# Optimization experiments

Hardware: AMD Instinct MI355X
Metric: run time of the kernel (lower is better)

The kernel has to match this reference:

```python
import jax, jax.numpy as jnp
import numpy as np

N_LOW, N_HIGH = 8000, 50000
C_IN, R2 = 25, 25
N_L25 = N_LOW * R2
E_LL, E_LH, E_HH = 32000, N_HIGH * 25, N_HIGH * 16
EPS = 1e-5


def _bn(x, g, b):
    # geometric_nn.BatchNorm in train mode: per-batch (per-node-set) stats
    mu = x.mean(0)
    var = x.var(0)
    return (x - mu) * jax.lax.rsqrt(var + EPS) * g + b


def _gcn(x, src, dst, W, b, n):
    # PyG GCNConv (normalize=True, add_self_loops=True) applied per-variable.
    # x: [n, V, C], W: [V, C, O]
    h = jnp.einsum('nvc,vco->nvo', x, W)
    sl = jnp.arange(n, dtype=src.dtype)
    s = jnp.concatenate([src, sl])
    d = jnp.concatenate([dst, sl])
    deg = jax.ops.segment_sum(jnp.ones_like(d, dtype=h.dtype), d, n)
    dis = jax.lax.rsqrt(jnp.maximum(deg, 1.0))
    norm = dis[s] * dis[d]
    out = jax.ops.segment_sum(h[s] * norm[:, None, None], d, n)
    return out + b


def _gatv2(xs, xd, src, dst, Wl, bl, Wr, br, att, bias, heads, oc, n_dst,
           concat, self_loops):
    # PyG GATv2Conv, eval mode (dropout off), aggr='mean'.
    hl = (xs @ Wl + bl).reshape(-1, heads, oc)  # source/messages
    hr = (xd @ Wr + br).reshape(-1, heads, oc)  # target/query
    if self_loops:
        sl = jnp.arange(n_dst, dtype=src.dtype)
        src = jnp.concatenate([src, sl])
        dst = jnp.concatenate([dst, sl])
    e = jax.nn.leaky_relu(hl[src] + hr[dst], 0.2)          # [E,H,C]
    logit = jnp.einsum('ehc,hc->eh', e, att)               # [E,H]
    m = jax.ops.segment_max(logit, dst, n_dst)
    a = jnp.exp(logit - m[dst])
    den = jax.ops.segment_sum(a, dst, n_dst)
    alpha = a / jnp.maximum(den, 1e-16)[dst]               # segment softmax
    msg = alpha[..., None] * hl[src]                       # [E,H,C]
    ssum = jax.ops.segment_sum(msg, dst, n_dst)
    cnt = jax.ops.segment_sum(jnp.ones_like(dst, dtype=ssum.dtype), dst, n_dst)
    out = ssum / jnp.maximum(cnt, 1.0)[:, None, None]      # mean aggregation
    out = out.reshape(n_dst, heads * oc) if concat else out.mean(1)
    return out + bias


def _forward(x_low, z_std, gcn_w, gcn_b, th_wl, th_bl, th_wr, th_br, th_att,
             th_bias, bn0_g, bn0_b, g1_wl, g1_bl, g1_wr, g1_br, g1_att,
             g1_bias, bn_g, bn_b, gm_wl, gm_bl, gm_wr, gm_br, gm_att, gm_bias,
             g5_wl, g5_bl, g5_wr, g5_br, g5_att, g5_bias, p_w1, p_b1, p_w2,
             p_b2, p_w3, p_b3, ei_ll, src_l2h, dst_l2h, ei_hh):
    # 5 GCN downscale branches done together: [N_LOW, 5, 625]
    enc = _gcn(x_low, ei_ll[0], ei_ll[1], gcn_w, gcn_b, N_LOW)
    # PixelShuffle(r=5) on [N,1,625,1,1] -> [N,1,25,5,5]; flatten+permute+cat
    # == reshape to [n, var, chan25, spat25] -> [n, spat25, var, chan25]
    enc = enc.reshape(N_LOW, 5, C_IN, R2).transpose(0, 3, 1, 2)
    enc = enc.reshape(N_L25, 5 * C_IN)                     # [200000, 125]
    h = _gatv2(enc, z_std, src_l2h, dst_l2h, th_wl, th_bl, th_wr, th_br,
               th_att, th_bias, 4, 25, N_HIGH, False, False)
    x = jnp.concatenate([z_std, h], axis=-1)               # [N_HIGH, 26]
    src, dst = ei_hh[0], ei_hh[1]
    x = _bn(x, bn0_g, bn0_b)
    x = _gatv2(x, x, src, dst, g1_wl, g1_bl, g1_wr, g1_br, g1_att, g1_bias,
               2, 64, N_HIGH, True, True)
    for i in range(3):
        x = jax.nn.relu(_bn(x, bn_g[i], bn_b[i]))
        x = _gatv2(x, x, src, dst, gm_wl[i], gm_bl[i], gm_wr[i], gm_br[i],
                   gm_att[i], gm_bias[i], 2, 64, N_HIGH, True, True)
    x = jax.nn.relu(_bn(x, bn_g[3], bn_b[3]))
    x = jax.nn.relu(_gatv2(x, x, src, dst, g5_wl, g5_bl, g5_wr, g5_br,
                           g5_att, g5_bias, 1, 64, N_HIGH, True, True))
    x = jax.nn.relu(x @ p_w1 + p_b1)
    x = jax.nn.relu(x @ p_w2 + p_b2)
    return x @ p_w3 + p_b3                                 # [N_HIGH, 1]


def setup_inputs() -> dict:
    key = jax.random.key(0)
    ks = iter(jax.random.split(key, 64))
    rn = lambda *s: jax.random.normal(next(ks), s, jnp.float32)
    w = lambda *s: rn(*s) * 0.1
    return dict(
        x_low=rn(N_LOW, 5, C_IN),
        z_std=rn(N_HIGH, 1),
        gcn_w=w(5, C_IN, C_IN * R2), gcn_b=w(5, C_IN * R2),
        th_wl=w(125, 100), th_bl=w(100), th_wr=w(1, 100), th_br=w(100),
        th_att=w(4, 25), th_bias=w(25),
        bn0_g=jnp.ones(26), bn0_b=jnp.zeros(26),
        g1_wl=w(26, 128), g1_bl=w(128), g1_wr=w(26, 128), g1_br=w(128),
        g1_att=w(2, 64), g1_bias=w(128),
        bn_g=jnp.ones((4, 128)), bn_b=jnp.zeros((4, 128)),
        gm_wl=w(3, 128, 128), gm_bl=w(3, 128), gm_wr=w(3, 128, 128),
        gm_br=w(3, 128), gm_att=w(3, 2, 64), gm_bias=w(3, 128),
        g5_wl=w(128, 64), g5_bl=w(64), g5_wr=w(128, 64), g5_br=w(64),
        g5_att=w(1, 64), g5_bias=w(64),
        p_w1=w(64, 64), p_b1=w(64), p_w2=w(64, 32), p_b2=w(32),
        p_w3=w(32, 1), p_b3=w(1),
        ei_ll=jax.random.randint(next(ks), (2, E_LL), 0, N_LOW, jnp.int32),
        src_l2h=jax.random.randint(next(ks), (E_LH,), 0, N_L25, jnp.int32),
        dst_l2h=jax.random.randint(next(ks), (E_LH,), 0, N_HIGH, jnp.int32),
        ei_hh=jax.random.randint(next(ks), (2, E_HH), 0, N_HIGH, jnp.int32),
    )


def reference(x_low, z_std, gcn_w, gcn_b, th_wl, th_bl, th_wr, th_br, th_att,
              th_bias, bn0_g, bn0_b, g1_wl, g1_bl, g1_wr, g1_br, g1_att,
              g1_bias, bn_g, bn_b, gm_wl, gm_bl, gm_wr, gm_br, gm_att,
              gm_bias, g5_wl, g5_bl, g5_wr, g5_br, g5_att, g5_bias, p_w1,
              p_b1, p_w2, p_b2, p_w3, p_b3, ei_ll, src_l2h, dst_l2h, ei_hh):
    return _forward(x_low, z_std, gcn_w, gcn_b, th_wl, th_bl, th_wr, th_br,
                    th_att, th_bias, bn0_g, bn0_b, g1_wl, g1_bl, g1_wr,
                    g1_br, g1_att, g1_bias, bn_g, bn_b, gm_wl, gm_bl, gm_wr,
                    gm_br, gm_att, gm_bias, g5_wl, g5_bl, g5_wr, g5_br,
                    g5_att, g5_bias, p_w1, p_b1, p_w2, p_b2, p_w3, p_b3,
                    ei_ll, src_l2h, dst_l2h, ei_hh)
```

## Files before the change

### kernel.cpp

```cpp
#include <hip/hip_runtime.h>

#define NLOW  8000
#define NHIGH 50000
#define NL25  200000
#define ELL   32000
#define ELH   1250000
#define EHH   800000

__global__ void k_fill_out(float* __restrict__ o, int n, float v) {
  int i = blockIdx.x * 256 + threadIdx.x;
  if (i < n) o[i] = v;
}

__global__ void k_init_deg(float* __restrict__ deg) {
  int i = blockIdx.x * 256 + threadIdx.x;
  if (i < NLOW) deg[i] = 1.0f;
}
__global__ void k_gcn_deg(const int* __restrict__ ei, float* __restrict__ deg) {
  int e = blockIdx.x * 256 + threadIdx.x;
  if (e >= ELL) return;
  int d = ei[ELL + e];
  if (d >= 0 && d < NLOW) atomicAdd(&deg[d], 1.0f);
}
__global__ void k_xa_init(const float* __restrict__ x, const float* __restrict__ deg,
                          float* __restrict__ xa) {
  int i = blockIdx.x * 256 + threadIdx.x;
  if (i >= NLOW * 125) return;
  xa[i] = x[i] / deg[i / 125];
}
__global__ void k_xa_edge(const float* __restrict__ x, const int* __restrict__ ei,
                          const float* __restrict__ deg, float* __restrict__ xa) {
  int gid = blockIdx.x * 256 + threadIdx.x;
  if (gid >= ELL * 125) return;
  int e = gid / 125, k = gid - e * 125;
  int s = ei[e], d = ei[ELL + e];
  if (s < 0 || s >= NLOW || d < 0 || d >= NLOW) return;
  float nrm = rsqrtf(deg[s]) * rsqrtf(deg[d]);
  atomicAdd(&xa[d * 125 + k], nrm * x[s * 125 + k]);
}
__global__ void k_prep_M(const float* __restrict__ W, const float* __restrict__ Wl,
                         float* __restrict__ M) {
  int gid = blockIdx.x * 256 + threadIdx.x;
  if (gid >= 125 * 2500) return;
  int vk = gid / 2500, r = gid - vk * 2500, sp = r / 100, j = r - sp * 100;
  int v = vk / 25;
  float acc = 0.f;
#pragma unroll
  for (int c = 0; c < 25; c++)
    acc = fmaf(W[vk * 625 + c * 25 + sp], Wl[(v * 25 + c) * 100 + j], acc);
  M[gid] = acc;
}
__global__ void k_prep_b2(const float* __restrict__ b, const float* __restrict__ Wl,
                          const float* __restrict__ bl, float* __restrict__ b2) {
  int gid = blockIdx.x * 256 + threadIdx.x;
  if (gid >= 2500) return;
  int sp = gid / 100, j = gid - sp * 100;
  float acc = bl[j];
  for (int v = 0; v < 5; v++)
#pragma unroll
    for (int c = 0; c < 25; c++)
      acc = fmaf(b[v * 625 + c * 25 + sp], Wl[(v * 25 + c) * 100 + j], acc);
  b2[gid] = acc;
}

__global__ void k_hlT_gemm(const float* __restrict__ A, const float* __restrict__ M,
                           const float* __restrict__ b2v, int pass,
                           float* __restrict__ out) {
  __shared__ float As[32 * 68];
  __shared__ float Bs[32 * 68];
  int t = threadIdx.x;
  int tx = t & 15, ty = t >> 4;
  int row0 = blockIdx.x * 64, col0 = blockIdx.y * 64;
  float acc[4][4];
#pragma unroll
  for (int i = 0; i < 4; i++)
#pragma unroll
    for (int j = 0; j < 4; j++) acc[i][j] = 0.f;
  for (int k0 = 0; k0 < 125; k0 += 32) {
    int kw = 125 - k0; if (kw > 32) kw = 32;
    for (int l = t; l < 64 * 32; l += 256) {
      int r = l >> 5, kk = l & 31;
      As[kk * 68 + r] = (kk < kw) ? A[(size_t)(row0 + r) * 125 + k0 + kk] : 0.f;
    }
    for (int l = t; l < 32 * 64; l += 256) {
      int kk = l >> 6, bb = l & 63;
      int b = col0 + bb;
      float v = 0.f;
      if (kk < kw && b < 1250) {
        int cm = (b / 50) * 100 + 50 * pass + (b % 50);
        v = M[(size_t)(k0 + kk) * 2500 + cm];
      }
      Bs[kk * 68 + bb] = v;
    }
    __syncthreads();
#pragma unroll 8
    for (int kk = 0; kk < 32; kk++) {
      float4 a4 = *(const float4*)&As[kk * 68 + ty * 4];
      float4 b4 = *(const float4*)&Bs[kk * 68 + tx * 4];
      float a[4] = {a4.x, a4.y, a4.z, a4.w};
      float b[4] = {b4.x, b4.y, b4.z, b4.w};
#pragma unroll
      for (int i = 0; i < 4; i++)
#pragma unroll
        for (int j = 0; j < 4; j++) acc[i][j] = fmaf(a[i], b[j], acc[i][j]);
    }
    __syncthreads();
  }
#pragma unroll
  for (int i = 0; i < 4; i++) {
    int r = row0 + ty * 4 + i;
#pragma unroll
    for (int j = 0; j < 4; j++) {
      int b = col0 + tx * 4 + j;
      if (b < 1250) {
        int cm = (b / 50) * 100 + 50 * pass + (b % 50);
        out[(size_t)r * 1250 + b] = acc[i][j] + b2v[cm];
      }
    }
  }
}

template <int CIN, bool BN, bool INRELU, bool OUTRELU>
__global__ void k_gemm_lin(const float* __restrict__ X, const float* __restrict__ sc,
                           const float* __restrict__ sh, const float* __restrict__ W,
                           const float* __restrict__ bias, float* __restrict__ out,
                           int n, int COUT) {
  __shared__ float As[32 * 68];
  __shared__ float Bs[32 * 68];
  int t = threadIdx.x;
  int tx = t & 15, ty = t >> 4;
  int row0 = blockIdx.x * 64, col0 = blockIdx.y * 64;
  float acc[4][4];
#pragma unroll
  for (int i = 0; i < 4; i++)
#pragma unroll
    for (int j = 0; j < 4; j++) acc[i][j] = 0.f;
  for (int k0 = 0; k0 < CIN; k0 += 32) {
    int kw = CIN - k0; if (kw > 32) kw = 32;
    for (int l = t; l < 64 * 32; l += 256) {
      int r = l >> 5, kk = l & 31;
      float v = 0.f;
      int rr = row0 + r;
      if (kk < kw && rr < n) {
        int k = k0 + kk;
        v = X[(size_t)rr * CIN + k];
        if (BN) v = fmaf(v, sc[k], sh[k]);
        if (INRELU) v = fmaxf(v, 0.f);
      }
      As[kk * 68 + r] = v;
    }
    for (int l = t; l < 32 * 64; l += 256) {
      int kk = l >> 6, cc = l & 63;
      Bs[kk * 68 + cc] = (kk < kw) ? W[(size_t)(k0 + kk) * COUT + col0 + cc] : 0.f;
    }
    __syncthreads();
#pragma unroll 8
    for (int kk = 0; kk < 32; kk++) {
      float4 a4 = *(const float4*)&As[kk * 68 + ty * 4];
      float4 b4 = *(const float4*)&Bs[kk * 68 + tx * 4];
      float a[4] = {a4.x, a4.y, a4.z, a4.w};
      float b[4] = {b4.x, b4.y, b4.z, b4.w};
#pragma unroll
      for (int i = 0; i < 4; i++)
#pragma unroll
        for (int j = 0; j < 4; j++) acc[i][j] = fmaf(a[i], b[j], acc[i][j]);
    }
    __syncthreads();
  }
#pragma unroll
  for (int i = 0; i < 4; i++) {
    int r = row0 + ty * 4 + i;
    if (r >= n) continue;
#pragma unroll
    for (int j = 0; j < 4; j++) {
      int c = col0 + tx * 4 + j;
      float v = acc[i][j] + bias[c];
      if (OUTRELU) v = fmaxf(v, 0.f);
      out[(size_t)r * COUT + c] = v;
    }
  }
}

__global__ void k_hist(const int* __restrict__ dst, int E, int* __restrict__ cnt) {
  int e = blockIdx.x * 256 + threadIdx.x;
  if (e >= E) return;
  int d = dst[e];
  if (d >= 0 && d < NHIGH) atomicAdd(&cnt[d], 1);
}
__global__ void k_scan1(const int* __restrict__ cnt, int* __restrict__ rp,
                        int* __restrict__ part, int N) {
  __shared__ int sh[256];
  int i = blockIdx.x * 256 + threadIdx.x;
  int v = (i < N) ? cnt[i] : 0;
  sh[threadIdx.x] = v;
  __syncthreads();
  for (int off = 1; off < 256; off <<= 1) {
    int t = (threadIdx.x >= off) ? sh[threadIdx.x - off] : 0;
    __syncthreads();
    sh[threadIdx.x] += t;
    __syncthreads();
  }
  if (i < N) rp[i] = sh[threadIdx.x] - v;
  if (threadIdx.x == 255) part[blockIdx.x] = sh[255];
}
__global__ void k_scan2(int* __restrict__ part, int nb) {
  __shared__ int sh[256];
  int v = (threadIdx.x < nb) ? part[threadIdx.x] : 0;
  sh[threadIdx.x] = v;
  __syncthreads();
  for (int off = 1; off < 256; off <<= 1) {
    int t = (threadIdx.x >= off) ? sh[threadIdx.x - off] : 0;
    __syncthreads();
    sh[threadIdx.x] += t;
    __syncthreads();
  }
  if (threadIdx.x < nb) part[threadIdx.x] = sh[threadIdx.x] - v;
}
__global__ void k_scan3(int* __restrict__ rp, const int* __restrict__ part, int N, int E) {
  int i = blockIdx.x * 256 + threadIdx.x;
  if (i < N) rp[i] += part[i / 256];
  if (i == 0) rp[N] = E;
}
__global__ void k_csr_scatter(const int* __restrict__ src, const int* __restrict__ dst,
                              const int* __restrict__ rp, int* __restrict__ fil,
                              int* __restrict__ col, int E) {
  int e = blockIdx.x * 256 + threadIdx.x;
  if (e >= E) return;
  int d = dst[e];
  if (d < 0 || d >= NHIGH) return;
  int pos = rp[d] + atomicAdd(&fil[d], 1);
  if (pos >= 0 && pos < E) col[pos] = src[e];
}

__global__ void k_gat_th2(const float* __restrict__ hl50, const float* __restrict__ z,
                          const float* __restrict__ wr, const float* __restrict__ br,
                          const float* __restrict__ att, const int* __restrict__ rp,
                          const int* __restrict__ col, int pass,
                          float* __restrict__ acc25) {
  int d = blockIdx.x, lane = threadIdx.x;
  int beg = rp[d];
  int deg = rp[d + 1] - beg;
  if (beg < 0) beg = 0;
  if (deg < 0) deg = 0;
  if (beg + deg > ELH) deg = (ELH - beg > 0) ? (ELH - beg) : 0;
  float zd = z[d];
  int g = lane >> 5, cc = lane & 31;
  bool act = cc < 25;
  int ch = g * 25 + (act ? cc : 0);
  float hrv = 0.f, atv = 0.f;
  if (act) {
    int j = 50 * pass + ch;
    hrv = fmaf(zd, wr[j], br[j]);
    atv = att[j];
  }
  float m = -3.0e38f, den = 0.f, acc = 0.f;
  for (int i = 0; i < deg; i++) {
    int s = col[beg + i];
    if (s < 0 || s >= NL25) s = 0;
    float r = act ? hl50[(size_t)s * 50 + ch] : 0.f;
    float e = r + hrv;
    e = (e > 0.f) ? e : 0.2f * e;
    float p = act ? e * atv : 0.f;
#pragma unroll
    for (int off = 16; off > 0; off >>= 1) p += __shfl_xor(p, off, 64);
    if (p > m) {
      float s_ = expf(m - p);
      den = fmaf(den, s_, 1.f);
      acc = fmaf(acc, s_, r);
      m = p;
    } else {
      float w_ = expf(p - m);
      den += w_;
      acc = fmaf(w_, r, acc);
    }
  }
  float v = acc / fmaxf(den, 1e-16f);
  float other = __shfl_down(v, 32, 64);
  if (lane < 25) {
    float contrib = v + other;
    if (pass == 0) acc25[d * 25 + lane] = contrib;
    else           acc25[d * 25 + lane] += contrib;
  }
}
__global__ void k_th_fin(const float* __restrict__ acc25, const int* __restrict__ rp,
                         const float* __restrict__ bias, const float* __restrict__ z,
                         float* __restrict__ x26) {
  int gid = blockIdx.x * 256 + threadIdx.x;
  int node = gid / 26, j = gid - node * 26;
  if (node >= NHIGH) return;
  if (j == 0) {
    x26[node * 26] = z[node];
  } else {
    int dg = rp[node + 1] - rp[node];
    if (dg < 1) dg = 1;
    x26[node * 26 + j] = acc25[node * 25 + j - 1] / (4.0f * (float)dg) + bias[j - 1];
  }
}

template <bool RELU>
__global__ void k_gat_hh2(const float* __restrict__ hl, const float* __restrict__ hr,
                          const float* __restrict__ att, const float* __restrict__ bias,
                          const int* __restrict__ rp, const int* __restrict__ col,
                          float* __restrict__ out) {
  const int F = 128;
  int d = blockIdx.x, lane = threadIdx.x;
  int h = lane >> 5, l2 = lane & 31;
  int c0 = h * 64 + l2, c1 = c0 + 32;
  int beg = rp[d];
  int deg = rp[d + 1] - beg;
  if (beg < 0) beg = 0;
  if (deg < 0) deg = 0;
  if (beg + deg > EHH) deg = (EHH - beg > 0) ? (EHH - beg) : 0;
  int tot = deg + 1;
  float hrv0 = hr[(size_t)d * F + c0], hrv1 = hr[(size_t)d * F + c1];
  float atv0 = att[c0], atv1 = att[c1];
  float m = -3.0e38f, den = 0.f, acc0 = 0.f, acc1 = 0.f;
  for (int i = 0; i < tot; i++) {
    int s = (i < deg) ? col[beg + i] : d;
    if (s < 0 || s >= NHIGH) s = 0;
    const float* row = hl + (size_t)s * F;
    float r0 = row[c0], r1 = row[c1];
    float e0 = r0 + hrv0; e0 = (e0 > 0.f) ? e0 : 0.2f * e0;
    float e1 = r1 + hrv1; e1 = (e1 > 0.f) ? e1 : 0.2f * e1;
    float p = fmaf(e0, atv0, e1 * atv1);
#pragma unroll
    for (int off = 16; off > 0; off >>= 1) p += __shfl_xor(p, off, 64);
    if (p > m) {
      float s_ = expf(m - p);
      den = fmaf(den, s_, 1.f);
      acc0 = fmaf(acc0, s_, r0);
      acc1 = fmaf(acc1, s_, r1);
      m = p;
    } else {
      float w_ = expf(p - m);
      den += w_;
      acc0 = fmaf(w_, r0, acc0);
      acc1 = fmaf(w_, r1, acc1);
    }
  }
  float inv = 1.0f / (fmaxf(den, 1e-16f) * (float)tot);
  float v0 = acc0 * inv + bias[c0];
  float v1 = acc1 * inv + bias[c1];
  if (RELU) { v0 = fmaxf(v0, 0.f); v1 = fmaxf(v1, 0.f); }
  out[(size_t)d * F + c0] = v0;
  out[(size_t)d * F + c1] = v1;
}
template <bool RELU>
__global__ void k_gat_hh1(const float* __restrict__ hl, const float* __restrict__ hr,
                          const float* __restrict__ att, const float* __restrict__ bias,
                          const int* __restrict__ rp, const int* __restrict__ col,
                          float* __restrict__ out) {
  const int F = 64;
  int d = blockIdx.x, lane = threadIdx.x;
  int beg = rp[d];
  int deg = rp[d + 1] - beg;
  if (beg < 0) beg = 0;
  if (deg < 0) deg = 0;
  if (beg + deg > EHH) deg = (EHH - beg > 0) ? (EHH - beg) : 0;
  int tot = deg + 1;
  float hrv = hr[(size_t)d * F + lane];
  float atv = att[lane];
  float m = -3.0e38f, den = 0.f, acc = 0.f;
  for (int i = 0; i < tot; i++) {
    int s = (i < deg) ? col[beg + i] : d;
    if (s < 0 || s >= NHIGH) s = 0;
    float r = hl[(size_t)s * F + lane];
    float e = r + hrv;
    e = (e > 0.f) ? e : 0.2f * e;
    float p = e * atv;
#pragma unroll
    for (int off = 32; off > 0; off >>= 1) p += __shfl_xor(p, off, 64);
    if (p > m) {
      float s_ = expf(m - p);
      den = fmaf(den, s_, 1.f);
      acc = fmaf(acc, s_, r);
      m = p;
    } else {
      float w_ = expf(p - m);
      den += w_;
      acc = fmaf(w_, r, acc);
    }
  }
  float v = acc / (fmaxf(den, 1e-16f) * (float)tot) + bias[lane];
  if (RELU) v = fmaxf(v, 0.f);
  out[(size_t)d * F + lane] = v;
}

__global__ void k_bn_part(const float* __restrict__ x, int C, int tpc,
                          float* __restrict__ ps, float* __restrict__ ps2) {
  int gch = blockIdx.x, t = threadIdx.x;
  int c = t % C, sub = t / C;
  float s = 0.f, s2 = 0.f;
  if (sub < tpc) {
    for (int r = gch * 500 + sub; r < gch * 500 + 500; r += tpc) {
      float v = x[(size_t)r * C + c];
      s += v;
      s2 = fmaf(v, v, s2);
    }
  }
  __shared__ float ls[256], ls2[256];
  ls[t] = s; ls2[t] = s2;
  __syncthreads();
  if (t < C) {
    float a = 0.f, a2 = 0.f;
    for (int u = 0; u < tpc; u++) { a += ls[u * C + t]; a2 += ls2[u * C + t]; }
    ps[gch * C + t] = a;
    ps2[gch * C + t] = a2;
  }
}
__global__ void k_bn_fin(const float* __restrict__ ps, const float* __restrict__ ps2,
                         int C, float n, const float* __restrict__ g,
                         const float* __restrict__ b, float* __restrict__ sc,
                         float* __restrict__ sh) {
  int c = blockIdx.x, t = threadIdx.x;
  __shared__ double ds[128], ds2[128];
  double a = 0, a2 = 0;
  for (int q = t; q < 100; q += 128) { a += ps[q * C + c]; a2 += ps2[q * C + c]; }
  ds[t] = a; ds2[t] = a2;
  __syncthreads();
  for (int off = 64; off > 0; off >>= 1) {
    if (t < off) { ds[t] += ds[t + off]; ds2[t] += ds2[t + off]; }
    __syncthreads();
  }
  if (t == 0) {
    double m = ds[0] / n;
    double v = ds2[0] / n - m * m;
    if (v < 0) v = 0;
    float scale = g[c] * rsqrtf((float)v + 1e-5f);
    sc[c] = scale;
    sh[c] = b[c] - (float)m * scale;
  }
}

template <int CIN, int COUT, bool RELU>
__global__ void k_linear(const float* __restrict__ x, const float* __restrict__ W,
                         const float* __restrict__ b, float* __restrict__ y, int n) {
  long long gid = (long long)blockIdx.x * 256 + threadIdx.x;
  int node = (int)(gid / COUT);
  int j = (int)(gid - (long long)node * COUT);
  if (node >= n) return;
  const float* xr = x + (size_t)node * CIN;
  float acc = b[j];
#pragma unroll 4
  for (int k = 0; k < CIN; k++) acc = fmaf(xr[k], W[k * COUT + j], acc);
  if (RELU) acc = fmaxf(acc, 0.f);
  y[(size_t)node * COUT + j] = acc;
}

extern "C" void kernel_launch(void* const* d_in, const int* in_sizes, int n_in,
                              void* d_out, int out_size, void* d_ws, size_t ws_size,
                              hipStream_t stream) {
  auto nb = [](long long t) { return dim3((unsigned)((t + 255) / 256)); };
  static const int FSZ[38] = {
      1000000, 50000, 78125, 3125, 12500, 100, 100, 100, 100, 25, 26, 26,
      3328, 128, 3328, 128, 128, 128, 512, 512, 49152, 384, 49152, 384, 384,
      384, 8192, 64, 8192, 64, 64, 64, 4096, 64, 2048, 32, 32, 1};
  static const int ISZ[4] = {64000, 1250000, 1250000, 1600000};
  if (n_in != 42) {
    k_fill_out<<<nb(out_size), 256, 0, stream>>>((float*)d_out, out_size, 500000.0f);
    return;
  }
  bool szok = true;
  for (int i = 0; i < 38; i++) szok &= (in_sizes[i] == FSZ[i]);
  for (int i = 0; i < 4; i++) szok &= (in_sizes[38 + i] == ISZ[i]);
  if (!szok) {
    k_fill_out<<<nb(out_size), 256, 0, stream>>>((float*)d_out, out_size, 600000.0f);
    return;
  }
  const size_t REQUIRED = 20146000ull * 4ull;
  if (ws_size < REQUIRED) {
    hipMemsetAsync(d_out, 0, (size_t)out_size * 4, stream);
    return;
  }

  const float* w[38];
  for (int i = 0; i < 38; i++) w[i] = (const float*)d_in[i];
  const int* ei_ll = (const int*)d_in[38];
  const int* s_l2h = (const int*)d_in[39];
  const int* d_l2h = (const int*)d_in[40];
  const int* ei_hh = (const int*)d_in[41];

  float* ws = (float*)d_ws;
  float* S0 = ws;
  float* S1 = ws + 6400000;
  float* S2 = ws + 12800000;
  float* hl50  = ws;
  float* acc25 = ws + 10000000;
  int*  rpT  = (int*)(ws + 11300000);
  int*  filT = (int*)(ws + 11360000);
  int*  colT = (int*)(ws + 11450000);
  float* xa  = ws + 12800000;
  float* Mt  = ws + 13800000;
  float* b2  = ws + 14112500;
  float* x26 = ws + 14200000;
  int*  rpH  = (int*)(ws + 19200000);
  int*  filH = (int*)(ws + 19260000);
  int*  colH = (int*)(ws + 19310000);
  float* deg = ws + 20110000;
  float* sc  = ws + 20118000;
  float* sh  = ws + 20118128;
  int*  part = (int*)(ws + 20118256);
  float* ps   = ws + 20120000;
  float* ps2  = ws + 20132800;

  auto build_csr = [&](const int* src, const int* dst, int E, int* rp, int* fil,
                       int* col) {
    hipMemsetAsync(fil, 0, NHIGH * 4, stream);
    k_hist<<<nb(E), 256, 0, stream>>>(dst, E, fil);
    int nblk = (NHIGH + 255) / 256;
    k_scan1<<<nblk, 256, 0, stream>>>(fil, rp, part, NHIGH);
    k_scan2<<<1, 256, 0, stream>>>(part, nblk);
    k_scan3<<<nb(NHIGH), 256, 0, stream>>>(rp, part, NHIGH, E);
    hipMemsetAsync(fil, 0, NHIGH * 4, stream);
    k_csr_scatter<<<nb(E), 256, 0, stream>>>(src, dst, rp, fil, col, E);
  };
  build_csr(s_l2h, d_l2h, ELH, rpT, filT, colT);
  build_csr(ei_hh, ei_hh + EHH, EHH, rpH, filH, colH);

  k_init_deg<<<nb(NLOW), 256, 0, stream>>>(deg);
  k_gcn_deg<<<nb(ELL), 256, 0, stream>>>(ei_ll, deg);
  k_xa_init<<<nb(NLOW * 125), 256, 0, stream>>>(w[0], deg, xa);
  k_xa_edge<<<nb((long long)ELL * 125), 256, 0, stream>>>(w[0], ei_ll, deg, xa);
  k_prep_M<<<nb(125 * 2500), 256, 0, stream>>>(w[2], w[4], Mt);
  k_prep_b2<<<nb(2500), 256, 0, stream>>>(w[3], w[4], w[5], b2);

  for (int p = 0; p < 2; p++) {
    k_hlT_gemm<<<dim3(125, 20), 256, 0, stream>>>(xa, Mt, b2, p, hl50);
    k_gat_th2<<<NHIGH, 64, 0, stream>>>(hl50, w[1], w[6], w[7], w[8], rpT, colT, p,
                                        acc25);
  }
  k_th_fin<<<nb((long long)NHIGH * 26), 256, 0, stream>>>(acc25, rpT, w[9], w[1], x26);

  const dim3 g1(782, 2), g2(782, 1);

  k_bn_part<<<100, 256, 0, stream>>>(x26, 26, 9, ps, ps2);
  k_bn_fin<<<26, 128, 0, stream>>>(ps, ps2, 26, (float)NHIGH, w[10], w[11], sc, sh);
  k_gemm_lin<26, true, false, false><<<g1, 256, 0, stream>>>(
      x26, sc, sh, w[12], w[13], S0, NHIGH, 128);
  k_gemm_lin<26, true, false, false><<<g1, 256, 0, stream>>>(
      x26, sc, sh, w[14], w[15], S1, NHIGH, 128);
  k_gat_hh2<false><<<NHIGH, 64, 0, stream>>>(S0, S1, w[16], w[17], rpH, colH, S2);

  for (int i = 0; i < 3; i++) {
    k_bn_part<<<100, 256, 0, stream>>>(S2, 128, 2, ps, ps2);
    k_bn_fin<<<128, 128, 0, stream>>>(ps, ps2, 128, (float)NHIGH, w[18] + i * 128,
                                      w[19] + i * 128, sc, sh);
    k_gemm_lin<128, true, true, false><<<g1, 256, 0, stream>>>(
        S2, sc, sh, w[20] + i * 16384, w[21] + i * 128, S0, NHIGH, 128);
    k_gemm_lin<128, true, true, false><<<g1, 256, 0, stream>>>(
        S2, sc, sh, w[22] + i * 16384, w[23] + i * 128, S1, NHIGH, 128);
    k_gat_hh2<false><<<NHIGH, 64, 0, stream>>>(S0, S1, w[24] + i * 128,
                                               w[25] + i * 128, rpH, colH, S2);
  }

  k_bn_part<<<100, 256, 0, stream>>>(S2, 128, 2, ps, ps2);
  k_bn_fin<<<128, 128, 0, stream>>>(ps, ps2, 128, (float)NHIGH, w[18] + 384,
                                    w[19] + 384, sc, sh);
  k_gemm_lin<128, true, true, false><<<g2, 256, 0, stream>>>(
      S2, sc, sh, w[26], w[27], S0, NHIGH, 64);
  k_gemm_lin<128, true, true, false><<<g2, 256, 0, stream>>>(
      S2, sc, sh, w[28], w[29], S1, NHIGH, 64);
  k_gat_hh1<true><<<NHIGH, 64, 0, stream>>>(S0, S1, w[30], w[31], rpH, colH, S2);

  k_gemm_lin<64, false, false, true><<<g2, 256, 0, stream>>>(
      S2, sc, sh, w[32], w[33], S0, NHIGH, 64);
  k_linear<64, 32, true><<<nb((long long)NHIGH * 32), 256, 0, stream>>>(
      S0, w[34], w[35], S1, NHIGH);
  k_linear<32, 1, false><<<nb((long long)NHIGH), 256, 0, stream>>>(
      S1, w[36], w[37], (float*)d_out, NHIGH);
}
```

Measured before the change: 1.843 ms.

## Store theta-layer messages in bf16 and batch two edges per shuffle reduction

```diff
diff --git a/kernel.cpp b/kernel.cpp
--- a/kernel.cpp
+++ b/kernel.cpp
@@ -1,4 +1,5 @@
 #include <hip/hip_runtime.h>
+#include <hip/hip_bf16.h>
 
 #define NLOW  8000
 #define NHIGH 50000
@@ -64,8 +65,8 @@
 }
 
 __global__ void k_hlT_gemm(const float* __restrict__ A, const float* __restrict__ M,
-                           const float* __restrict__ b2v, int pass,
-                           float* __restrict__ out) {
+                           const float* __restrict__ b2v,
+                           unsigned short* __restrict__ out16) {
   __shared__ float As[32 * 68];
   __shared__ float Bs[32 * 68];
   int t = threadIdx.x;
@@ -86,8 +87,10 @@
       int kk = l >> 6, bb = l & 63;
       int b = col0 + bb;
       float v = 0.f;
-      if (kk < kw && b < 1250) {
-        int cm = (b / 50) * 100 + 50 * pass + (b % 50);
+      if (kk < kw && b < 2500) {
+        int sp = b / 100, r = b - sp * 100;
+        int g = r / 50, q = r - g * 50, cc = q >> 1, hp = q & 1;
+        int cm = sp * 100 + (2 * g + hp) * 25 + cc;
         v = M[(size_t)(k0 + kk) * 2500 + cm];
       }
       Bs[kk * 68 + bb] = v;
@@ -112,9 +115,12 @@
 #pragma unroll
     for (int j = 0; j < 4; j++) {
       int b = col0 + tx * 4 + j;
-      if (b < 1250) {
-        int cm = (b / 50) * 100 + 50 * pass + (b % 50);
-        out[(size_t)r * 1250 + b] = acc[i][j] + b2v[cm];
+      if (b < 2500) {
+        int sp = b / 100, rr = b - sp * 100;
+        int g = rr / 50, q = rr - g * 50, cc = q >> 1, hp = q & 1;
+        int cm = sp * 100 + (2 * g + hp) * 25 + cc;
+        __hip_bfloat16 hv = __float2bfloat16(acc[i][j] + b2v[cm]);
+        out16[(size_t)r * 2500 + b] = *(unsigned short*)&hv;
       }
     }
   }
@@ -232,11 +238,38 @@
   if (pos >= 0 && pos < E) col[pos] = src[e];
 }
 
-__global__ void k_gat_th2(const float* __restrict__ hl50, const float* __restrict__ z,
-                          const float* __restrict__ wr, const float* __restrict__ br,
-                          const float* __restrict__ att, const int* __restrict__ rp,
-                          const int* __restrict__ col, int pass,
-                          float* __restrict__ acc25) {
+__device__ __forceinline__ void osm2(float p, float r0, float r1, float& m,
+                                     float& den, float& a0, float& a1) {
+  if (p > m) {
+    float s_ = expf(m - p);
+    den = fmaf(den, s_, 1.f);
+    a0 = fmaf(a0, s_, r0);
+    a1 = fmaf(a1, s_, r1);
+    m = p;
+  } else {
+    float w_ = expf(p - m);
+    den += w_;
+    a0 = fmaf(w_, r0, a0);
+    a1 = fmaf(w_, r1, a1);
+  }
+}
+__device__ __forceinline__ void osm1(float p, float r, float& m, float& den, float& a) {
+  if (p > m) {
+    float s_ = expf(m - p);
+    den = fmaf(den, s_, 1.f);
+    a = fmaf(a, s_, r);
+    m = p;
+  } else {
+    float w_ = expf(p - m);
+    den += w_;
+    a = fmaf(w_, r, a);
+  }
+}
+
+__global__ void k_gat_th(const unsigned* __restrict__ hlu, const float* __restrict__ z,
+                         const float* __restrict__ wr, const float* __restrict__ br,
+                         const float* __restrict__ att, const int* __restrict__ rp,
+                         const int* __restrict__ col, float* __restrict__ acc25) {
   int d = blockIdx.x, lane = threadIdx.x;
   int beg = rp[d];
   int deg = rp[d + 1] - beg;
@@ -246,41 +279,38 @@
   float zd = z[d];
   int g = lane >> 5, cc = lane & 31;
   bool act = cc < 25;
-  int ch = g * 25 + (act ? cc : 0);
-  float hrv = 0.f, atv = 0.f;
+  int j0 = 50 * g + (act ? cc : 0), j1 = j0 + 25;
+  float hrv0 = 0.f, atv0 = 0.f, hrv1 = 0.f, atv1 = 0.f;
   if (act) {
-    int j = 50 * pass + ch;
-    hrv = fmaf(zd, wr[j], br[j]);
-    atv = att[j];
-  }
-  float m = -3.0e38f, den = 0.f, acc = 0.f;
+    hrv0 = fmaf(zd, wr[j0], br[j0]); atv0 = att[j0];
+    hrv1 = fmaf(zd, wr[j1], br[j1]); atv1 = att[j1];
+  }
+  bool hi = (lane & 16) != 0;
+  float m0 = -3.0e38f, den0 = 0.f, a0 = 0.f;
+  float m1 = -3.0e38f, den1 = 0.f, a1 = 0.f;
   for (int i = 0; i < deg; i++) {
     int s = col[beg + i];
     if (s < 0 || s >= NL25) s = 0;
-    float r = act ? hl50[(size_t)s * 50 + ch] : 0.f;
-    float e = r + hrv;
-    e = (e > 0.f) ? e : 0.2f * e;
-    float p = act ? e * atv : 0.f;
-#pragma unroll
-    for (int off = 16; off > 0; off >>= 1) p += __shfl_xor(p, off, 64);
-    if (p > m) {
-      float s_ = expf(m - p);
-      den = fmaf(den, s_, 1.f);
-      acc = fmaf(acc, s_, r);
-      m = p;
-    } else {
-      float w_ = expf(p - m);
-      den += w_;
-      acc = fmaf(w_, r, acc);
-    }
-  }
-  float v = acc / fmaxf(den, 1e-16f);
+    unsigned u = act ? hlu[(size_t)s * 50 + g * 25 + cc] : 0u;
+    float r0 = __uint_as_float(u << 16);
+    float r1 = __uint_as_float(u & 0xffff0000u);
+    float e0 = r0 + hrv0; e0 = (e0 > 0.f) ? e0 : 0.2f * e0;
+    float e1 = r1 + hrv1; e1 = (e1 > 0.f) ? e1 : 0.2f * e1;
+    float p0 = e0 * atv0, p1 = e1 * atv1;
+    float own = hi ? p1 : p0;
+    float oth = hi ? p0 : p1;
+    float q = own + __shfl_xor(oth, 16, 64);
+#pragma unroll
+    for (int off = 8; off > 0; off >>= 1) q += __shfl_xor(q, off, 64);
+    float o = __shfl_xor(q, 16, 64);
+    p0 = hi ? o : q;
+    p1 = hi ? q : o;
+    osm1(p0, r0, m0, den0, a0);
+    osm1(p1, r1, m1, den1, a1);
+  }
+  float v = a0 / fmaxf(den0, 1e-16f) + a1 / fmaxf(den1, 1e-16f);
   float other = __shfl_down(v, 32, 64);
-  if (lane < 25) {
-    float contrib = v + other;
-    if (pass == 0) acc25[d * 25 + lane] = contrib;
-    else           acc25[d * 25 + lane] += contrib;
-  }
+  if (lane < 25) acc25[d * 25 + lane] = v + other;
 }
 __global__ void k_th_fin(const float* __restrict__ acc25, const int* __restrict__ rp,
                          const float* __restrict__ bias, const float* __restrict__ z,
@@ -314,8 +344,36 @@
   int tot = deg + 1;
   float hrv0 = hr[(size_t)d * F + c0], hrv1 = hr[(size_t)d * F + c1];
   float atv0 = att[c0], atv1 = att[c1];
+  bool hi = (lane & 16) != 0;
   float m = -3.0e38f, den = 0.f, acc0 = 0.f, acc1 = 0.f;
-  for (int i = 0; i < tot; i++) {
+  int i = 0;
+  for (; i + 2 <= tot; i += 2) {
+    int sA = (i < deg) ? col[beg + i] : d;
+    int sB = (i + 1 < deg) ? col[beg + i + 1] : d;
+    if (sA < 0 || sA >= NHIGH) sA = 0;
+    if (sB < 0 || sB >= NHIGH) sB = 0;
+    const float* rowA = hl + (size_t)sA * F;
+    const float* rowB = hl + (size_t)sB * F;
+    float r0a = rowA[c0], r1a = rowA[c1];
+    float r0b = rowB[c0], r1b = rowB[c1];
+    float e0a = r0a + hrv0; e0a = (e0a > 0.f) ? e0a : 0.2f * e0a;
+    float e1a = r1a + hrv1; e1a = (e1a > 0.f) ? e1a : 0.2f * e1a;
+    float pA = fmaf(e0a, atv0, e1a * atv1);
+    float e0b = r0b + hrv0; e0b = (e0b > 0.f) ? e0b : 0.2f * e0b;
+    float e1b = r1b + hrv1; e1b = (e1b > 0.f) ? e1b : 0.2f * e1b;
+    float pB = fmaf(e0b, atv0, e1b * atv1);
+    float own = hi ? pB : pA;
+    float oth = hi ? pA : pB;
+    float q = own + __shfl_xor(oth, 16, 64);
+#pragma unroll
+    for (int off = 8; off > 0; off >>= 1) q += __shfl_xor(q, off, 64);
+    float o = __shfl_xor(q, 16, 64);
+    pA = hi ? o : q;
+    pB = hi ? q : o;
+    osm2(pA, r0a, r1a, m, den, acc0, acc1);
+    osm2(pB, r0b, r1b, m, den, acc0, acc1);
+  }
+  if (i < tot) {
     int s = (i < deg) ? col[beg + i] : d;
     if (s < 0 || s >= NHIGH) s = 0;
     const float* row = hl + (size_t)s * F;
@@ -325,18 +383,7 @@
     float p = fmaf(e0, atv0, e1 * atv1);
 #pragma unroll
     for (int off = 16; off > 0; off >>= 1) p += __shfl_xor(p, off, 64);
-    if (p > m) {
-      float s_ = expf(m - p);
-      den = fmaf(den, s_, 1.f);
-      acc0 = fmaf(acc0, s_, r0);
-      acc1 = fmaf(acc1, s_, r1);
-      m = p;
-    } else {
-      float w_ = expf(p - m);
-      den += w_;
-      acc0 = fmaf(w_, r0, acc0);
-      acc1 = fmaf(w_, r1, acc1);
-    }
+    osm2(p, r0, r1, m, den, acc0, acc1);
   }
   float inv = 1.0f / (fmaxf(den, 1e-16f) * (float)tot);
   float v0 = acc0 * inv + bias[c0];
@@ -360,26 +407,39 @@
   int tot = deg + 1;
   float hrv = hr[(size_t)d * F + lane];
   float atv = att[lane];
+  bool hi = lane >= 32;
   float m = -3.0e38f, den = 0.f, acc = 0.f;
-  for (int i = 0; i < tot; i++) {
+  int i = 0;
+  for (; i + 2 <= tot; i += 2) {
+    int sA = (i < deg) ? col[beg + i] : d;
+    int sB = (i + 1 < deg) ? col[beg + i + 1] : d;
+    if (sA < 0 || sA >= NHIGH) sA = 0;
+    if (sB < 0 || sB >= NHIGH) sB = 0;
+    float rA = hl[(size_t)sA * F + lane];
+    float rB = hl[(size_t)sB * F + lane];
+    float eA = rA + hrv; eA = (eA > 0.f) ? eA : 0.2f * eA;
+    float eB = rB + hrv; eB = (eB > 0.f) ? eB : 0.2f * eB;
+    float pA = eA * atv, pB = eB * atv;
+    float own = hi ? pB : pA;
+    float oth = hi ? pA : pB;
+    float q = own + __shfl_xor(oth, 32, 64);
+#pragma unroll
+    for (int off = 16; off > 0; off >>= 1) q += __shfl_xor(q, off, 64);
+    float o = __shfl_xor(q, 32, 64);
+    pA = hi ? o : q;
+    pB = hi ? q : o;
+    osm1(pA, rA, m, den, acc);
+    osm1(pB, rB, m, den, acc);
+  }
+  if (i < tot) {
     int s = (i < deg) ? col[beg + i] : d;
     if (s < 0 || s >= NHIGH) s = 0;
     float r = hl[(size_t)s * F + lane];
-    float e = r + hrv;
-    e = (e > 0.f) ? e : 0.2f * e;
+    float e = r + hrv; e = (e > 0.f) ? e : 0.2f * e;
     float p = e * atv;
 #pragma unroll
     for (int off = 32; off > 0; off >>= 1) p += __shfl_xor(p, off, 64);
-    if (p > m) {
-      float s_ = expf(m - p);
-      den = fmaf(den, s_, 1.f);
-      acc = fmaf(acc, s_, r);
-      m = p;
-    } else {
-      float w_ = expf(p - m);
-      den += w_;
-      acc = fmaf(w_, r, acc);
-    }
+    osm1(p, r, m, den, acc);
   }
   float v = acc / (fmaxf(den, 1e-16f) * (float)tot) + bias[lane];
   if (RELU) v = fmaxf(v, 0.f);
@@ -484,7 +544,7 @@
   float* S0 = ws;
   float* S1 = ws + 6400000;
   float* S2 = ws + 12800000;
-  float* hl50  = ws;
+  unsigned short* hl100 = (unsigned short*)ws;
   float* acc25 = ws + 10000000;
   int*  rpT  = (int*)(ws + 11300000);
   int*  filT = (int*)(ws + 11360000);
@@ -524,11 +584,9 @@
   k_prep_M<<<nb(125 * 2500), 256, 0, stream>>>(w[2], w[4], Mt);
   k_prep_b2<<<nb(2500), 256, 0, stream>>>(w[3], w[4], w[5], b2);
 
-  for (int p = 0; p < 2; p++) {
-    k_hlT_gemm<<<dim3(125, 20), 256, 0, stream>>>(xa, Mt, b2, p, hl50);
-    k_gat_th2<<<NHIGH, 64, 0, stream>>>(hl50, w[1], w[6], w[7], w[8], rpT, colT, p,
-                                        acc25);
-  }
+  k_hlT_gemm<<<dim3(125, 40), 256, 0, stream>>>(xa, Mt, b2, hl100);
+  k_gat_th<<<NHIGH, 64, 0, stream>>>((const unsigned*)hl100, w[1], w[6], w[7], w[8],
+                                     rpT, colT, acc25);
   k_th_fin<<<nb((long long)NHIGH * 26), 256, 0, stream>>>(acc25, rpT, w[9], w[1], x26);
 
   const dim3 g1(782, 2), g2(782, 1);
```

Result: faster. 1.657 ms (-10.1%).
